# Performance work log

Measured on AMD Instinct MI355X. Metric: run time of the kernel, lower is better.

The kernel has to match this reference:

```python
import jax, jax.numpy as jnp
import numpy as np
from jax import lax

L, B, H, Z, V = 64, 32, 256, 256, 32000  # steps, max_ast_depth, hidden=units, latent, vocab


def setup_inputs() -> dict:
    key = jax.random.key(0)
    ks = jax.random.split(key, 32)
    p = lambda i, shape: jax.random.normal(ks[i], shape, dtype=jnp.float32) * 0.05
    inp = {
        "nodes": jax.random.randint(ks[0], (L, B), 0, V),
        "edges": jax.random.randint(ks[1], (L, B), 0, 2) > 0,
        "enc_init": jax.random.normal(ks[2], (B, H), dtype=jnp.float32) * 0.001,
        "eps": jax.random.normal(ks[3], (B, Z), dtype=jnp.float32),
        "emb": p(4, (V, H)),
    }
    for j, n in enumerate(["enc_c", "enc_s", "dec_c", "dec_s"]):
        inp[n + "_Wih"] = p(5 + 4 * j, (3 * H, H))
        inp[n + "_Whh"] = p(6 + 4 * j, (3 * H, H))
        inp[n + "_bih"] = p(7 + 4 * j, (3 * H,))
        inp[n + "_bhh"] = p(8 + 4 * j, (3 * H,))
    inp["W_mean"] = p(21, (Z, H)); inp["b_mean"] = p(22, (Z,))
    inp["W_logv"] = p(23, (Z, H)); inp["b_logv"] = p(24, (Z,))
    inp["W_l2h"] = p(25, (H, Z)); inp["b_l2h"] = p(26, (H,))
    inp["W_voc"] = p(27, (V, H)); inp["b_voc"] = p(28, (V,))
    return inp


def _gru_cell(Wih, Whh, bih, bhh, x, h):
    # torch.nn.GRU single-layer cell; x, h: [B, H]
    gi = x @ Wih.T + bih
    gh = h @ Whh.T + bhh
    ir, iz, inn = jnp.split(gi, 3, axis=-1)
    hr, hz, hn = jnp.split(gh, 3, axis=-1)
    r = jax.nn.sigmoid(ir + hr)
    zg = jax.nn.sigmoid(iz + hz)
    n = jnp.tanh(inn + r * hn)
    return (1.0 - zg) * n + zg * h


def _tree_rnn(pc, ps, emb_nodes, edges, h0):
    # emb_nodes: [L, B, H], edges: [L, B] bool, h0: [B, H]
    # each step runs child & sibling GRUs on the SAME state, selects per node by edge
    def step(h, xe):
        x, e = xe
        hc = _gru_cell(*pc, x, h)
        hs = _gru_cell(*ps, x, h)
        h_new = jnp.where(e[:, None], hc, hs)
        return h_new, h_new  # 1-layer GRU, seq_len 1: output == new state
    h_final, outs = lax.scan(step, h0, (emb_nodes, edges))
    return outs, h_final  # outs: [L, B, H]


def reference(nodes, edges, enc_init, eps, emb,
              enc_c_Wih, enc_c_Whh, enc_c_bih, enc_c_bhh,
              enc_s_Wih, enc_s_Whh, enc_s_bih, enc_s_bhh,
              dec_c_Wih, dec_c_Whh, dec_c_bih, dec_c_bhh,
              dec_s_Wih, dec_s_Whh, dec_s_bih, dec_s_bhh,
              W_mean, b_mean, W_logv, b_logv, W_l2h, b_l2h, W_voc, b_voc):
    x = emb[nodes]  # [L, B, H]
    _, h_enc = _tree_rnn((enc_c_Wih, enc_c_Whh, enc_c_bih, enc_c_bhh),
                         (enc_s_Wih, enc_s_Whh, enc_s_bih, enc_s_bhh),
                         x, edges, enc_init)
    mean = h_enc @ W_mean.T + b_mean          # [B, Z]
    logv = h_enc @ W_logv.T + b_logv
    z = eps * jnp.exp(0.5 * logv) + mean      # reparameterization
    h0 = z @ W_l2h.T + b_l2h                  # decoder initial state [B, H]
    outs, _ = _tree_rnn((dec_c_Wih, dec_c_Whh, dec_c_bih, dec_c_bhh),
                        (dec_s_Wih, dec_s_Whh, dec_s_bih, dec_s_bhh),
                        x, edges, h0)         # [L, B, H]
    logits = outs @ W_voc.T + b_voc           # [L, B, V]
    logp = jax.nn.log_softmax(logits, axis=-1)
    return logp, mean, logv, z
```

## Files before the change

### kernel.cpp

```cpp
#include <hip/hip_runtime.h>
#include <stdint.h>

typedef unsigned short u16;
typedef unsigned int u32;

#define L_STEPS 64
#define B_SZ 32
#define H_SZ 256
#define Z_SZ 256
#define V_SZ 32000
#define H2 128
#define G3H 768

typedef _Float16 h2_t __attribute__((ext_vector_type(2)));

#define WHH2_OFF   0
#define WIH2_OFF   393216
#define WM2_OFF    786432
#define WLV2_OFF   819200
#define WL2H2_OFF  851968
#define GI2_OFF    884736
#define OUTS2_OFF  4030464

#define OUT_MEAN_OFF  65536000
#define OUT_LOGV_OFF  65544192
#define OUT_Z_OFF     65552384

__device__ __forceinline__ float fdot2(h2_t a, h2_t b, float c){
#if __has_builtin(__builtin_amdgcn_fdot2)
  return __builtin_amdgcn_fdot2(a, b, c, false);
#else
  return c + (float)a.x*(float)b.x + (float)a.y*(float)b.y;
#endif
}
__device__ __forceinline__ float sigm(float x){ return 1.f/(1.f + __expf(-x)); }

struct PackTArgs { const float2* src[11]; int n_h2[11]; int dstoff[11]; };

__global__ __launch_bounds__(256) void k_packt(PackTArgs p, h2_t* wsh){
  int m = blockIdx.y;
  int r = blockIdx.x*256 + threadIdx.x;
  if (r >= p.n_h2[m]) return;
  int row = r >> 7, k2 = r & 127;
  float2 f = p.src[m][r];
  h2_t h; h.x = (_Float16)f.x; h.y = (_Float16)f.y;
  int off = (((row>>6)*32 + (k2>>2))*64 + (row&63))*4 + (k2&3);
  wsh[p.dstoff[m] + off] = h;
}

struct GiArgs { const float* bih[4]; };

__global__ __launch_bounds__(256) void k_gi(const int* __restrict__ nodes,
                                            const float* __restrict__ emb,
                                            const h2_t* __restrict__ wih2,
                                            GiArgs ga, h2_t* __restrict__ gi2){
  int l = blockIdx.x, g = blockIdx.y, t = threadIdx.x;
  __shared__ __align__(16) h2_t x2[B_SZ*132];
  #pragma unroll
  for (int it=0; it<16; ++it){
    int lin = it*256 + t;
    int bb = lin >> 7, k2 = lin & 127;
    int node = nodes[l*B_SZ + bb];
    float2 f = ((const float2*)(emb + (size_t)node*H_SZ))[k2];
    h2_t r; r.x=(_Float16)f.x; r.y=(_Float16)f.y;
    x2[bb*132 + k2] = r;
  }
  __syncthreads();
  const float* bih = ga.bih[g];
  for (int jc=0; jc<3; ++jc){
    int j = jc*256 + t;
    float acc[32];
    #pragma unroll
    for (int bb=0;bb<32;bb++) acc[bb]=0.f;
    const float4* Wv = (const float4*)wih2 + (size_t)g*24576 + (j>>6)*2048 + (j&63);
    #pragma unroll 2
    for (int kb=0;kb<32;kb++){
      union{float4 f; h2_t h[4];} w4;
      w4.f = Wv[kb*64];
      #pragma unroll
      for (int kc=0;kc<4;kc++){
        h2_t w = w4.h[kc];
        int k2 = kb*4 + kc;
        #pragma unroll
        for (int bb=0;bb<32;bb++) acc[bb] = fdot2(x2[bb*132+k2], w, acc[bb]);
      }
    }
    float bvv = bih[j];
    int base = (g*2048 + l*B_SZ)*384 + (j>>1);
    #pragma unroll
    for (int bb=0;bb<32;bb++){
      float own = acc[bb] + bvv;
      float oth = __shfl_xor(own, 1, 64);
      if (!(t&1)){
        h2_t r; r.x=(_Float16)own; r.y=(_Float16)oth;
        gi2[base + bb*384] = r;
      }
    }
  }
}

struct ScanArgs {
  const float* bhh[4];
  const float* b_mean; const float* b_logv; const float* b_l2h;
  const float* enc_init; const float* eps;
};

__global__ __launch_bounds__(768) void k_scan(const int* __restrict__ edges, ScanArgs sa,
                                              const h2_t* __restrict__ wsh,
                                              h2_t* __restrict__ outs2,
                                              float* __restrict__ out){
  int b = blockIdx.x, t = threadIdx.x;
  int i = t & 255, gate = t >> 8;
  int lane = t & 63, rb = t >> 6;
  __shared__ float h_lds[H_SZ];
  __shared__ __align__(16) h2_t hs2[H2];
  __shared__ float g_lds[512];
  __shared__ float s_bhh[4*G3H];
  __shared__ int s_edge[L_STEPS];
  const _Float16* gi_all = (const _Float16*)(wsh + GI2_OFF);

  if (t < H_SZ) h_lds[t] = sa.enc_init[b*H_SZ + t];
  if (t < L_STEPS) s_edge[t] = edges[t*B_SZ + b];
  #pragma unroll
  for (int m=0;m<4;m++) s_bhh[m*G3H + t] = sa.bhh[m][t];
  __syncthreads();
  if (t < H2){ h2_t r; r.x=(_Float16)h_lds[2*t]; r.y=(_Float16)h_lds[2*t+1]; hs2[t]=r; }
  __syncthreads();

  const float4* hsv = (const float4*)hs2;

  for (int ph=0; ph<2; ++ph){
    for (int l=0; l<L_STEPS; ++l){
      int e = s_edge[l];
      int gsel = (ph ? 2 : 0) + (e ? 0 : 1);
      float gi0=0.f, gi1=0.f, gi2v=0.f;
      if (t < H_SZ){
        const _Float16* gr = gi_all + (size_t)(gsel*2048 + l*B_SZ + b)*G3H;
        gi0  = (float)gr[i];
        gi1  = (float)gr[256+i];
        gi2v = (float)gr[512+i];
      }
      float bv = s_bhh[gsel*G3H + t];
      const float4* Wv = (const float4*)wsh + (size_t)gsel*24576 + rb*2048 + lane;
      float a0=0.f,a1=0.f,a2=0.f,a3=0.f;
      #pragma unroll 8
      for (int kb=0;kb<32;kb++){
        union{float4 f; h2_t h[4];} w, x;
        w.f = Wv[kb*64];
        x.f = hsv[kb];
        a0 = fdot2(x.h[0], w.h[0], a0);
        a1 = fdot2(x.h[1], w.h[1], a1);
        a2 = fdot2(x.h[2], w.h[2], a2);
        a3 = fdot2(x.h[3], w.h[3], a3);
      }
      float acc = (a0+a1)+(a2+a3) + bv;
      if (gate) g_lds[(gate-1)*256 + i] = acc;
      __syncthreads();
      if (t < H_SZ){
        float r = sigm(gi0 + acc);
        float z = sigm(gi1 + g_lds[i]);
        float n = tanhf(gi2v + r*g_lds[256+i]);
        float hn = (1.f - z)*n + z*h_lds[i];
        h_lds[i] = hn;
        float ho = __shfl_xor(hn, 1, 64);
        if (!(i & 1)){
          h2_t pk; pk.x=(_Float16)hn; pk.y=(_Float16)ho;
          hs2[i>>1] = pk;
          if (ph) outs2[(l*B_SZ + b)*H2 + (i>>1)] = pk;
        }
      }
      __syncthreads();
    }

    if (ph == 0){
      if (t < H_SZ){
        const float4* WmV = (const float4*)(wsh + WM2_OFF)  + (t>>6)*2048 + (t&63);
        const float4* WlV = (const float4*)(wsh + WLV2_OFF) + (t>>6)*2048 + (t&63);
        float m0=0.f,m1=0.f,m2=0.f,m3=0.f, l0=0.f,l1=0.f,l2=0.f,l3=0.f;
        #pragma unroll 8
        for (int kb=0;kb<32;kb++){
          union{float4 f; h2_t h[4];} wm, wl, x;
          x.f  = hsv[kb];
          wm.f = WmV[kb*64];
          wl.f = WlV[kb*64];
          m0=fdot2(x.h[0],wm.h[0],m0); m1=fdot2(x.h[1],wm.h[1],m1);
          m2=fdot2(x.h[2],wm.h[2],m2); m3=fdot2(x.h[3],wm.h[3],m3);
          l0=fdot2(x.h[0],wl.h[0],l0); l1=fdot2(x.h[1],wl.h[1],l1);
          l2=fdot2(x.h[2],wl.h[2],l2); l3=fdot2(x.h[3],wl.h[3],l3);
        }
        float am = (m0+m1)+(m2+m3) + sa.b_mean[t];
        float al = (l0+l1)+(l2+l3) + sa.b_logv[t];
        float zv = sa.eps[b*Z_SZ + t] * __expf(0.5f*al) + am;
        out[OUT_MEAN_OFF + b*Z_SZ + t] = am;
        out[OUT_LOGV_OFF + b*Z_SZ + t] = al;
        out[OUT_Z_OFF    + b*Z_SZ + t] = zv;
        h_lds[t] = zv;
      }
      __syncthreads();
      if (t < H2){ h2_t r; r.x=(_Float16)h_lds[2*t]; r.y=(_Float16)h_lds[2*t+1]; hs2[t]=r; }
      __syncthreads();
      float h0v = 0.f;
      if (t < H_SZ){
        const float4* WzV = (const float4*)(wsh + WL2H2_OFF) + (t>>6)*2048 + (t&63);
        float z0=0.f,z1=0.f,z2=0.f,z3=0.f;
        #pragma unroll 8
        for (int kb=0;kb<32;kb++){
          union{float4 f; h2_t h[4];} w, x;
          x.f = hsv[kb];
          w.f = WzV[kb*64];
          z0=fdot2(x.h[0],w.h[0],z0); z1=fdot2(x.h[1],w.h[1],z1);
          z2=fdot2(x.h[2],w.h[2],z2); z3=fdot2(x.h[3],w.h[3],z3);
        }
        h0v = (z0+z1)+(z2+z3) + sa.b_l2h[t];
      }
      __syncthreads();
      if (t < H_SZ) h_lds[t] = h0v;
      __syncthreads();
      if (t < H2){ h2_t r; r.x=(_Float16)h_lds[2*t]; r.y=(_Float16)h_lds[2*t+1]; hs2[t]=r; }
      __syncthreads();
    }
  }
}

__global__ __launch_bounds__(512) void k_gemm(const h2_t* __restrict__ outs2,
                                              const float* __restrict__ wv,
                                              const float* __restrict__ bvoc,
                                              float* __restrict__ outf){
  int t = threadIdx.x;
  int vq = t & 31, rq = t >> 5;
  int Nb = blockIdx.x * 256, Mb = blockIdx.y * 128;
  __shared__ __align__(16) h2_t A[16*128];
  __shared__ __align__(16) h2_t Bs[16*256];
  float acc[8][8];
  #pragma unroll
  for (int a=0;a<8;a++){
    #pragma unroll
    for (int c=0;c<8;c++) acc[a][c]=0.f;
  }

  for (int kc=0;kc<8;kc++){
    {
      int r = t >> 2, q = t & 3;
      union{float4 f; h2_t h[4];} u;
      u.f = ((const float4*)(outs2 + (Mb + r)*H2 + kc*16))[q];
      #pragma unroll
      for (int uu=0; uu<4; ++uu) A[(q*4+uu)*128 + r] = u.h[uu];
    }
    {
      int v = t >> 1, q = t & 1;
      const float* wrow = wv + (size_t)(Nb + v)*H_SZ + kc*32 + q*16;
      #pragma unroll
      for (int p=0;p<4;p++){
        float4 f = ((const float4*)wrow)[p];
        h2_t h0; h0.x=(_Float16)f.x; h0.y=(_Float16)f.y;
        h2_t h1; h1.x=(_Float16)f.z; h1.y=(_Float16)f.w;
        Bs[(q*8+p*2  )*256 + v] = h0;
        Bs[(q*8+p*2+1)*256 + v] = h1;
      }
    }
    __syncthreads();
    #pragma unroll 2
    for (int k2=0;k2<16;k2++){
      union{float4 f; h2_t h[4];} a0, a1, b0, b1;
      a0.f = *(const float4*)(A  + k2*128 + rq*8);
      a1.f = *(const float4*)(A  + k2*128 + rq*8 + 4);
      b0.f = *(const float4*)(Bs + k2*256 + vq*4);
      b1.f = *(const float4*)(Bs + k2*256 + vq*4 + 128);
      #pragma unroll
      for (int ii=0;ii<8;ii++){
        h2_t av = (ii<4)? a0.h[ii] : a1.h[ii-4];
        #pragma unroll
        for (int jj=0;jj<8;jj++){
          h2_t bv = (jj<4)? b0.h[jj] : b1.h[jj-4];
          acc[ii][jj] = fdot2(av, bv, acc[ii][jj]);
        }
      }
    }
    __syncthreads();
  }

  float bias0[4], bias1[4];
  #pragma unroll
  for (int jj=0;jj<4;jj++){
    bias0[jj] = bvoc[Nb + 4*vq + jj];
    bias1[jj] = bvoc[Nb + 128 + 4*vq + jj];
  }
  #pragma unroll
  for (int ii=0;ii<8;ii++){
    size_t base = (size_t)(Mb + rq*8 + ii)*(size_t)V_SZ + (size_t)Nb;
    float4 o0, o1;
    o0.x = acc[ii][0]+bias0[0]; o0.y = acc[ii][1]+bias0[1];
    o0.z = acc[ii][2]+bias0[2]; o0.w = acc[ii][3]+bias0[3];
    o1.x = acc[ii][4]+bias1[0]; o1.y = acc[ii][5]+bias1[1];
    o1.z = acc[ii][6]+bias1[2]; o1.w = acc[ii][7]+bias1[3];
    *(float4*)(outf + base + 4*vq)       = o0;
    *(float4*)(outf + base + 128 + 4*vq) = o1;
  }
}

__global__ __launch_bounds__(256) void k_softmax(float* __restrict__ outf){
  int rrow = blockIdx.x, t = threadIdx.x;
  float4* row = (float4*)(outf + (size_t)rrow * V_SZ);
  float4 v[32];
  #pragma unroll
  for (int i=0;i<31;i++) v[i] = row[i*256 + t];
  if (t < 64) v[31] = row[7936 + t];
  else { v[31].x = -1e30f; v[31].y = -1e30f; v[31].z = -1e30f; v[31].w = -1e30f; }

  float m = -1e30f;
  #pragma unroll
  for (int i=0;i<32;i++) m = fmaxf(m, fmaxf(fmaxf(v[i].x, v[i].y), fmaxf(v[i].z, v[i].w)));

  __shared__ float sred[4];
  __shared__ float sbc;
  int wid = t >> 6, lane = t & 63;
  #pragma unroll
  for (int o=32;o;o>>=1) m = fmaxf(m, __shfl_xor(m, o, 64));
  if (lane==0) sred[wid] = m;
  __syncthreads();
  if (t==0) sbc = fmaxf(fmaxf(sred[0],sred[1]), fmaxf(sred[2],sred[3]));
  __syncthreads();
  m = sbc;
  __syncthreads();

  float s = 0.f;
  #pragma unroll
  for (int i=0;i<32;i++){
    s += __expf(v[i].x - m) + __expf(v[i].y - m) + __expf(v[i].z - m) + __expf(v[i].w - m);
  }
  #pragma unroll
  for (int o=32;o;o>>=1) s += __shfl_xor(s, o, 64);
  if (lane==0) sred[wid] = s;
  __syncthreads();
  if (t==0) sbc = sred[0]+sred[1]+sred[2]+sred[3];
  __syncthreads();
  float lse = m + logf(sbc);

  #pragma unroll
  for (int i=0;i<31;i++){
    v[i].x -= lse; v[i].y -= lse; v[i].z -= lse; v[i].w -= lse;
    row[i*256 + t] = v[i];
  }
  if (t < 64){
    v[31].x -= lse; v[31].y -= lse; v[31].z -= lse; v[31].w -= lse;
    row[7936 + t] = v[31];
  }
}

extern "C" void kernel_launch(void* const* d_in, const int* in_sizes, int n_in,
                              void* d_out, int out_size, void* d_ws, size_t ws_size,
                              hipStream_t stream){
  const int* nodes = (const int*)d_in[0];
  const int* edges = (const int*)d_in[1];
  h2_t* wsh = (h2_t*)d_ws;
  float* outf = (float*)d_out;

  PackTArgs pt;
  const int srcidx[11] = {6,10,14,18, 5,9,13,17, 21,23,25};
  for (int k=0;k<11;k++){
    pt.src[k] = (const float2*)d_in[srcidx[k]];
    pt.n_h2[k] = (k < 8) ? 98304 : 32768;
  }
  for (int k=0;k<4;k++) pt.dstoff[k]   = WHH2_OFF + k*98304;
  for (int k=0;k<4;k++) pt.dstoff[4+k] = WIH2_OFF + k*98304;
  pt.dstoff[8] = WM2_OFF; pt.dstoff[9] = WLV2_OFF; pt.dstoff[10] = WL2H2_OFF;
  k_packt<<<dim3(384,11), dim3(256), 0, stream>>>(pt, wsh);

  GiArgs ga;
  ga.bih[0]=(const float*)d_in[7];  ga.bih[1]=(const float*)d_in[11];
  ga.bih[2]=(const float*)d_in[15]; ga.bih[3]=(const float*)d_in[19];
  k_gi<<<dim3(64,4), dim3(256), 0, stream>>>(nodes, (const float*)d_in[4], wsh + WIH2_OFF, ga, wsh + GI2_OFF);

  ScanArgs sa;
  sa.bhh[0]=(const float*)d_in[8];  sa.bhh[1]=(const float*)d_in[12];
  sa.bhh[2]=(const float*)d_in[16]; sa.bhh[3]=(const float*)d_in[20];
  sa.b_mean=(const float*)d_in[22]; sa.b_logv=(const float*)d_in[24]; sa.b_l2h=(const float*)d_in[26];
  sa.enc_init=(const float*)d_in[2]; sa.eps=(const float*)d_in[3];
  k_scan<<<dim3(32), dim3(768), 0, stream>>>(edges, sa, wsh, wsh + OUTS2_OFF, outf);

  k_gemm<<<dim3(125,16), dim3(512), 0, stream>>>(wsh + OUTS2_OFF, (const float*)d_in[27], (const float*)d_in[28], outf);

  k_softmax<<<dim3(2048), dim3(256), 0, stream>>>(outf);
}
```

Measured before the change: 1.185 ms.

## Use MFMA f16 matrix cores for vocab projection GEMM with pre-packed fp16 weights

```diff
diff --git a/kernel.cpp b/kernel.cpp
--- a/kernel.cpp
+++ b/kernel.cpp
@@ -13,6 +13,8 @@
 #define G3H 768
 
 typedef _Float16 h2_t __attribute__((ext_vector_type(2)));
+typedef _Float16 f16x8 __attribute__((ext_vector_type(8)));
+typedef float f32x4 __attribute__((ext_vector_type(4)));
 
 #define WHH2_OFF   0
 #define WIH2_OFF   393216
@@ -21,6 +23,8 @@
 #define WL2H2_OFF  851968
 #define GI2_OFF    884736
 #define OUTS2_OFF  4030464
+#define W16_OFF    4292608
+#define WS_NEEDED  ((size_t)(W16_OFF + 4096000) * 4)
 
 #define OUT_MEAN_OFF  65536000
 #define OUT_LOGV_OFF  65544192
@@ -46,6 +50,15 @@
   h2_t h; h.x = (_Float16)f.x; h.y = (_Float16)f.y;
   int off = (((row>>6)*32 + (k2>>2))*64 + (row&63))*4 + (k2&3);
   wsh[p.dstoff[m] + off] = h;
+}
+
+__global__ __launch_bounds__(256) void k_packv(const float2* __restrict__ src,
+                                               h2_t* __restrict__ dst, int total){
+  int idx = blockIdx.x*256 + threadIdx.x;
+  if (idx >= total) return;
+  float2 f = src[idx];
+  h2_t h; h.x = (_Float16)f.x; h.y = (_Float16)f.y;
+  dst[idx] = h;
 }
 
 struct GiArgs { const float* bih[4]; };
@@ -222,6 +235,83 @@
   }
 }
 
+__global__ __launch_bounds__(256) void k_gemm2(const h2_t* __restrict__ outs2,
+                                               const _Float16* __restrict__ wv16,
+                                               const float* __restrict__ bvoc,
+                                               float* __restrict__ outf){
+  int t = threadIdx.x;
+  int lane = t & 63, w = t >> 6;
+  int wm = w & 1, wn = w >> 1;
+  int Mb = blockIdx.x * 64, Nb = blockIdx.y * 128;
+  int lr = lane & 15, lq = lane >> 4;
+
+  __shared__ __align__(16) _Float16 As[64*64];
+  __shared__ __align__(16) _Float16 Bs[128*64];
+
+  f32x4 acc[2][4];
+  #pragma unroll
+  for (int mi=0;mi<2;mi++)
+    #pragma unroll
+    for (int nj=0;nj<4;nj++) acc[mi][nj] = (f32x4){0.f,0.f,0.f,0.f};
+
+  for (int kc=0; kc<4; ++kc){
+    #pragma unroll
+    for (int q=0;q<2;q++){
+      int ch = q*256 + t;
+      int row = ch >> 3, kb = ch & 7;
+      float4 d = ((const float4*)(outs2 + (size_t)(Mb + row)*H2 + kc*32))[kb];
+      ((float4*)As)[row*8 + (kb ^ (row & 7))] = d;
+    }
+    #pragma unroll
+    for (int q=0;q<4;q++){
+      int ch = q*256 + t;
+      int row = ch >> 3, kb = ch & 7;
+      float4 d = ((const float4*)(wv16 + (size_t)(Nb + row)*H_SZ + kc*64))[kb];
+      ((float4*)Bs)[row*8 + (kb ^ (row & 7))] = d;
+    }
+    __syncthreads();
+    union{float4 f; f16x8 h;} af[2][2], bf[4][2];
+    #pragma unroll
+    for (int mi=0;mi<2;mi++)
+      #pragma unroll
+      for (int kk=0;kk<2;kk++){
+        int row = wm*32 + mi*16 + lr;
+        int ks = kk*4 + lq;
+        af[mi][kk].f = ((const float4*)As)[row*8 + (ks ^ (row & 7))];
+      }
+    #pragma unroll
+    for (int nj=0;nj<4;nj++)
+      #pragma unroll
+      for (int kk=0;kk<2;kk++){
+        int row = wn*64 + nj*16 + lr;
+        int ks = kk*4 + lq;
+        bf[nj][kk].f = ((const float4*)Bs)[row*8 + (ks ^ (row & 7))];
+      }
+    #pragma unroll
+    for (int kk=0;kk<2;kk++)
+      #pragma unroll
+      for (int mi=0;mi<2;mi++)
+        #pragma unroll
+        for (int nj=0;nj<4;nj++)
+          acc[mi][nj] = __builtin_amdgcn_mfma_f32_16x16x32_f16(
+                          af[mi][kk].h, bf[nj][kk].h, acc[mi][nj], 0, 0, 0);
+    __syncthreads();
+  }
+
+  #pragma unroll
+  for (int nj=0;nj<4;nj++){
+    int col = Nb + wn*64 + nj*16 + lr;
+    float bias = bvoc[col];
+    #pragma unroll
+    for (int mi=0;mi<2;mi++){
+      int r0 = Mb + wm*32 + mi*16 + lq*4;
+      #pragma unroll
+      for (int rg=0;rg<4;rg++)
+        outf[(size_t)(r0 + rg)*V_SZ + col] = acc[mi][nj][rg] + bias;
+    }
+  }
+}
+
 __global__ __launch_bounds__(512) void k_gemm(const h2_t* __restrict__ outs2,
                                               const float* __restrict__ wv,
                                               const float* __restrict__ bvoc,
@@ -230,7 +320,7 @@
   int vq = t & 31, rq = t >> 5;
   int Nb = blockIdx.x * 256, Mb = blockIdx.y * 128;
   __shared__ __align__(16) h2_t A[16*128];
-  __shared__ __align__(16) h2_t Bs[16*256];
+  __shared__ __align__(16) h2_t Bss[16*256];
   float acc[8][8];
   #pragma unroll
   for (int a=0;a<8;a++){
@@ -254,8 +344,8 @@
         float4 f = ((const float4*)wrow)[p];
         h2_t h0; h0.x=(_Float16)f.x; h0.y=(_Float16)f.y;
         h2_t h1; h1.x=(_Float16)f.z; h1.y=(_Float16)f.w;
-        Bs[(q*8+p*2  )*256 + v] = h0;
-        Bs[(q*8+p*2+1)*256 + v] = h1;
+        Bss[(q*8+p*2  )*256 + v] = h0;
+        Bss[(q*8+p*2+1)*256 + v] = h1;
       }
     }
     __syncthreads();
@@ -264,8 +354,8 @@
       union{float4 f; h2_t h[4];} a0, a1, b0, b1;
       a0.f = *(const float4*)(A  + k2*128 + rq*8);
       a1.f = *(const float4*)(A  + k2*128 + rq*8 + 4);
-      b0.f = *(const float4*)(Bs + k2*256 + vq*4);
-      b1.f = *(const float4*)(Bs + k2*256 + vq*4 + 128);
+      b0.f = *(const float4*)(Bss + k2*256 + vq*4);
+      b1.f = *(const float4*)(Bss + k2*256 + vq*4 + 128);
       #pragma unroll
       for (int ii=0;ii<8;ii++){
         h2_t av = (ii<4)? a0.h[ii] : a1.h[ii-4];
@@ -354,6 +444,7 @@
   const int* edges = (const int*)d_in[1];
   h2_t* wsh = (h2_t*)d_ws;
   float* outf = (float*)d_out;
+  bool mfma_path = (ws_size >= WS_NEEDED);
 
   PackTArgs pt;
   const int srcidx[11] = {6,10,14,18, 5,9,13,17, 21,23,25};
@@ -365,6 +456,10 @@
   for (int k=0;k<4;k++) pt.dstoff[4+k] = WIH2_OFF + k*98304;
   pt.dstoff[8] = WM2_OFF; pt.dstoff[9] = WLV2_OFF; pt.dstoff[10] = WL2H2_OFF;
   k_packt<<<dim3(384,11), dim3(256), 0, stream>>>(pt, wsh);
+
+  if (mfma_path)
+    k_packv<<<dim3(16000), dim3(256), 0, stream>>>((const float2*)d_in[27],
+                                                   wsh + W16_OFF, 4096000);
 
   GiArgs ga;
   ga.bih[0]=(const float*)d_in[7];  ga.bih[1]=(const float*)d_in[11];
@@ -378,7 +473,13 @@
   sa.enc_init=(const float*)d_in[2]; sa.eps=(const float*)d_in[3];
   k_scan<<<dim3(32), dim3(768), 0, stream>>>(edges, sa, wsh, wsh + OUTS2_OFF, outf);
 
-  k_gemm<<<dim3(125,16), dim3(512), 0, stream>>>(wsh + OUTS2_OFF, (const float*)d_in[27], (const float*)d_in[28], outf);
+  if (mfma_path)
+    k_gemm2<<<dim3(32,250), dim3(256), 0, stream>>>(wsh + OUTS2_OFF,
+                                                    (const _Float16*)(wsh + W16_OFF),
+                                                    (const float*)d_in[28], outf);
+  else
+    k_gemm<<<dim3(125,16), dim3(512), 0, stream>>>(wsh + OUTS2_OFF, (const float*)d_in[27],
+                                                   (const float*)d_in[28], outf);
 
   k_softmax<<<dim3(2048), dim3(256), 0, stream>>>(outf);
 }
```

Result: faster. 971.2 us (-18.0%).
